# Kernel tuning notes

Hardware: AMD Instinct MI355X
Metric: run time of the kernel (lower is better)

Reference implementation:

```python
import jax, jax.numpy as jnp
import numpy as np

B, N, C, H = 8, 8192, 256, 8  # batch, tokens, dim, heads


def setup_inputs() -> dict:
    key = jax.random.key(0)
    ks = jax.random.split(key, 12)
    p = lambda i, shape: jax.random.normal(ks[i], shape, jnp.float32) * 0.02
    return {
        "x0": jax.random.normal(ks[0], (B, N, C), jnp.float32),
        "x1": jax.random.normal(ks[1], (B, N, C), jnp.float32),
        # relation_judger MLP (shared by both directions)
        "fc1_w": p(2, (C, 2 * C)), "fc1_b": jnp.zeros((C,), jnp.float32),
        "fc2_w": p(3, (C, C)), "fc2_b": jnp.zeros((C,), jnp.float32),
        # cross_attn_0_to_1
        "in_w_01": p(4, (3 * C, C)), "in_b_01": jnp.zeros((3 * C,), jnp.float32),
        "out_w_01": p(5, (C, C)), "out_b_01": jnp.zeros((C,), jnp.float32),
        # cross_attn_1_to_0
        "in_w_10": p(6, (3 * C, C)), "in_b_10": jnp.zeros((3 * C,), jnp.float32),
        "out_w_10": p(7, (C, C)), "out_b_10": jnp.zeros((C,), jnp.float32),
        # noise embeddings (2 rows each)
        "k_noise": p(8, (2, C)), "v_noise": p(9, (2, C)),
    }


def _judge(a, b, fc1_w, fc1_b, fc2_w, fc2_b):
    # Mlp2(2C->C->C) + softmax over channels; torch GELU default = exact erf
    h = jax.nn.gelu(jnp.concatenate([a, b], axis=-1) @ fc1_w.T + fc1_b, approximate=False)
    return jax.nn.softmax(h @ fc2_w.T + fc2_b, axis=-1)


def _mha_kv2(q, k, v, Wi, bi, Wo, bo):
    # q: [B,N,C]; k,v: [B,N,2,C]. Each token attends over its own 2 kv slots
    # (matches torch MHA with batch_first=False, seq_q=1, seq_kv=2, batch=N).
    hd = C // H
    Q = (q @ Wi[:C].T + bi[:C]).reshape(B, N, H, hd)
    K = (k @ Wi[C:2 * C].T + bi[C:2 * C]).reshape(B, N, 2, H, hd)
    V = (v @ Wi[2 * C:].T + bi[2 * C:]).reshape(B, N, 2, H, hd)
    scores = jnp.einsum('bnhd,bnkhd->bnhk', Q, K) / jnp.sqrt(jnp.asarray(hd, q.dtype))
    attn = jax.nn.softmax(scores, axis=-1)  # [B,N,H,2]
    ctx = jnp.einsum('bnhk,bnkhd->bnhd', attn, V).reshape(B, N, C)
    return ctx @ Wo.T + bo


def reference(x0, x1, fc1_w, fc1_b, fc2_w, fc2_b,
              in_w_01, in_b_01, out_w_01, out_b_01,
              in_w_10, in_b_10, out_w_10, out_b_10,
              k_noise, v_noise):
    # noise expansion was under @torch.no_grad() -> detach noise weights
    kn = jax.lax.stop_gradient(k_noise)
    vn = jax.lax.stop_gradient(v_noise)

    rel01 = _judge(x0, x1, fc1_w, fc1_b, fc2_w, fc2_b)       # [B,N,C]
    k01 = jnp.stack([x0 + kn[0], x0 * rel01], axis=2)        # [B,N,2,C]
    v01 = jnp.stack([x0 + vn[0], x1], axis=2)
    out01 = _mha_kv2(x0, k01, v01, in_w_01, in_b_01, out_w_01, out_b_01)

    rel10 = _judge(x1, x0, fc1_w, fc1_b, fc2_w, fc2_b)
    k10 = jnp.stack([x1 + kn[1], x1 * rel10], axis=2)
    v10 = jnp.stack([x1 + vn[1], x0], axis=2)
    out10 = _mha_kv2(x1, k10, v10, in_w_10, in_b_10, out_w_10, out_b_10)

    return x0 + out01, x1 + out10
```

## Files before the change

kernel.cpp:

```cpp
#include <hip/hip_runtime.h>
#include <cstdint>
#include <cstddef>


#define BNv  65536
#define TBNv 131072
#define NCv  16777216ull

typedef __attribute__((ext_vector_type(4))) float  f32x4;
typedef __attribute__((ext_vector_type(8))) short  short8;
typedef __attribute__((ext_vector_type(4))) float  float4_t;
typedef __attribute__((ext_vector_type(4))) unsigned short ushort4_t;

__device__ __forceinline__ float b2f(unsigned short u) {
  unsigned int x = ((unsigned int)u) << 16;
  return __builtin_bit_cast(float, x);
}
__device__ __forceinline__ unsigned short f2b(float f) {
  unsigned int u = __builtin_bit_cast(unsigned int, f);
  unsigned int r = (u + 0x7fffu + ((u >> 16) & 1u)) >> 16;
  return (unsigned short)r;
}

__device__ __forceinline__ void async16(const void* g, void* l) {
  __builtin_amdgcn_global_load_lds(
      (const __attribute__((address_space(1))) void*)g,
      (__attribute__((address_space(3))) void*)l, 16, 0, 0);
}

__device__ __forceinline__ void mfma_loop(
    const unsigned short* __restrict__ A1,
    const unsigned short* __restrict__ A2,
    const unsigned short* __restrict__ W,
    int ldw, int koff2, int npairs,
    size_t Arow0, int Wrow0,
    unsigned short* Asm, unsigned short* Wsm,
    f32x4 (&acc)[4][4], int t)
{
  const int l  = t & 63;
  const int wv = t >> 6;
  const int wr = (wv >> 1) * 64;
  const int wc = (wv & 1) * 64;
  const int lr = l & 15;
  const int kcS = (((l >> 4) ^ ((lr >> 1) & 3)) * 8);

  const int srow  = t >> 2;
  const int scolS = (((t & 3) ^ ((t >> 3) & 3)) * 8);
  const int ldst  = t * 8;

  for (int p = 0; p < npairs; ++p) {
    const unsigned short* A = p ? A2 : A1;
    const int kb = p ? koff2 : 0;
    for (int kt = 0; kt < 8; ++kt) {
      const int k0 = kt * 32;
      __syncthreads();
      async16(&A[(Arow0 + srow) * 256 + (size_t)(k0 + scolS)],        &Asm[ldst]);
      async16(&A[(Arow0 + 64 + srow) * 256 + (size_t)(k0 + scolS)],   &Asm[64 * 32 + ldst]);
      async16(&W[(size_t)(Wrow0 + srow) * ldw + (kb + k0 + scolS)],      &Wsm[ldst]);
      async16(&W[(size_t)(Wrow0 + 64 + srow) * ldw + (kb + k0 + scolS)], &Wsm[64 * 32 + ldst]);
      __syncthreads();

      short8 af[4], bfr[4];
#pragma unroll
      for (int m = 0; m < 4; ++m)
        af[m] = *(const short8*)&Asm[(wr + m * 16 + lr) * 32 + kcS];
#pragma unroll
      for (int n = 0; n < 4; ++n)
        bfr[n] = *(const short8*)&Wsm[(wc + n * 16 + lr) * 32 + kcS];
#pragma unroll
      for (int m = 0; m < 4; ++m)
#pragma unroll
        for (int n = 0; n < 4; ++n)
          acc[m][n] = __builtin_amdgcn_mfma_f32_16x16x32_bf16(af[m], bfr[n], acc[m][n], 0, 0, 0);
    }
  }
}

template <int EPI>
__device__ __forceinline__ void store_tile(
    f32x4 (&acc)[4][4], int t,
    const float* __restrict__ bias,
    const float* __restrict__ res,
    void* __restrict__ outp,
    int ldo)
{
  const int l = t & 63, wv = t >> 6;
  const int wr = (wv >> 1) * 64, wc = (wv & 1) * 64;
  const int lr = l & 15, lq = l >> 4;
#pragma unroll
  for (int m = 0; m < 4; ++m) {
#pragma unroll
    for (int n = 0; n < 4; ++n) {
#pragma unroll
      for (int r = 0; r < 4; ++r) {
        int rowi = wr + m * 16 + lq * 4 + r;
        int coli = wc + n * 16 + lr;
        float v = acc[m][n][r] + bias[coli];
        if (EPI == 1)
          v = 0.5f * v * (1.0f + erff(v * 0.70710678118654752f));
        if (EPI == 2)
          ((float*)outp)[(size_t)rowi * ldo + coli] = v + res[(size_t)rowi * 256 + coli];
        else
          ((unsigned short*)outp)[(size_t)rowi * ldo + coli] = f2b(v);
      }
    }
  }
}

__global__ __launch_bounds__(256)
void gemm_mega(const unsigned short* __restrict__ xb,
               const unsigned short* __restrict__ Wcat0,
               const unsigned short* __restrict__ Wcat1,
               const unsigned short* __restrict__ wfc1,
               const float* __restrict__ bcat0,
               const float* __restrict__ bcat1,
               const float* __restrict__ fc1_b,
               unsigned short* __restrict__ qkv,
               unsigned short* __restrict__ v1b,
               unsigned short* __restrict__ hbuf)
{
  __shared__ unsigned short Asm[128 * 32];
  __shared__ unsigned short Wsm[128 * 32];
  const int t = threadIdx.x;

  const int nwg = 10240, BPC = 160;
  int bid  = blockIdx.x;
  int wgid = (bid & 7) * (nwg >> 3) + (bid >> 3);
  int chunk = wgid / BPC, rem = wgid % BPC;
  int x = chunk * 16 + rem / 10;
  int y = rem % 10;

  const int half = x >> 9;
  const size_t tok0 = (size_t)(x & 511) * 128;
  const unsigned short* A1 = xb + (size_t)half * (BNv * 256);

  f32x4 acc[4][4] = {};

  if (y < 8) {
    const unsigned short* W = half ? Wcat1 : Wcat0;
    const float* bias = (half ? bcat1 : bcat0) + y * 128;
    mfma_loop(A1, nullptr, W, 256, 0, 1, tok0, y * 128, Asm, Wsm, acc, t);
    if (y < 6) {
      size_t row0 = (size_t)half * BNv + tok0;
      store_tile<0>(acc, t, bias, nullptr, qkv + row0 * 768 + y * 128, 768);
    } else {
      size_t row0 = (size_t)(1 - half) * BNv + tok0;
      store_tile<0>(acc, t, bias, nullptr, v1b + row0 * 256 + (y - 6) * 128, 256);
    }
  } else {
    const unsigned short* A2 = xb + (size_t)(1 - half) * (BNv * 256);
    mfma_loop(A1, A2, wfc1, 512, 256, 2, tok0, (y - 8) * 128, Asm, Wsm, acc, t);
    size_t row0 = (size_t)half * BNv + tok0;
    store_tile<1>(acc, t, fc1_b + (y - 8) * 128, nullptr,
                  hbuf + row0 * 256 + (y - 8) * 128, 256);
  }
}

template <int EPI>
__global__ __launch_bounds__(256)
void gemm_b2(const unsigned short* __restrict__ A,
             const unsigned short* __restrict__ W0,
             const unsigned short* __restrict__ W1,
             const float* __restrict__ b0, const float* __restrict__ b1,
             const float* __restrict__ res0, const float* __restrict__ res1,
             void* __restrict__ outp)
{
  __shared__ unsigned short Asm[128 * 32];
  __shared__ unsigned short Wsm[128 * 32];
  const int t = threadIdx.x;

  const int nwg = 2048;
  int bid  = blockIdx.x;
  int wgid = (bid & 7) * (nwg >> 3) + (bid >> 3);
  int chunk = wgid >> 5, rem = wgid & 31;
  int x = chunk * 16 + (rem >> 1);
  int y = rem & 1;

  const int half = x >> 9;
  const size_t row0 = (size_t)x * 128;

  f32x4 acc[4][4] = {};
  mfma_loop(A, nullptr, half ? W1 : W0, 256, 0, 1, row0, y * 128, Asm, Wsm, acc, t);

  const float* bias = (half ? b1 : b0) + y * 128;
  if (EPI == 2) {
    const float* res = (half ? res1 : res0) + (row0 - (size_t)half * BNv) * 256 + y * 128;
    store_tile<2>(acc, t, bias, res, (float*)outp + row0 * 256 + y * 128, 256);
  } else {
    store_tile<0>(acc, t, bias, nullptr,
                  (unsigned short*)outp + row0 * 256 + y * 128, 256);
  }
}


__global__ __launch_bounds__(256)
void cvt_x(const float* __restrict__ x0, const float* __restrict__ x1,
           unsigned short* __restrict__ xb)
{
  size_t i = ((size_t)blockIdx.x * 256 + threadIdx.x) * 8;
  const float* s = (i < NCv) ? (x0 + i) : (x1 + (i - NCv));
  float4_t a = *(const float4_t*)s;
  float4_t b = *(const float4_t*)(s + 4);
  short8 o;
  o[0] = (short)f2b(a[0]); o[1] = (short)f2b(a[1]);
  o[2] = (short)f2b(a[2]); o[3] = (short)f2b(a[3]);
  o[4] = (short)f2b(b[0]); o[5] = (short)f2b(b[1]);
  o[6] = (short)f2b(b[2]); o[7] = (short)f2b(b[3]);
  *(short8*)(xb + i) = o;
}

__global__ __launch_bounds__(256)
void prep_w(const float* fc1_w, const float* fc2_w,
            const float* in_w01, const float* out_w01,
            const float* in_w10, const float* out_w10,
            unsigned short* wfc1, unsigned short* wfc2,
            unsigned short* Wcat0, unsigned short* Wcat1,
            unsigned short* wout0, unsigned short* wout1)
{
  const float* src; unsigned short* dst; int n;
  switch (blockIdx.y) {
    case 0: src = fc1_w;             dst = wfc1;             n = 131072; break;
    case 1: src = fc2_w;             dst = wfc2;             n = 65536;  break;
    case 2: src = in_w01;            dst = Wcat0;            n = 196608; break;
    case 3: src = in_w10 + 512*256;  dst = Wcat0 + 768*256;  n = 65536;  break;
    case 4: src = in_w10;            dst = Wcat1;            n = 196608; break;
    case 5: src = in_w01 + 512*256;  dst = Wcat1 + 768*256;  n = 65536;  break;
    case 6: src = out_w01;           dst = wout0;            n = 65536;  break;
    default: src = out_w10;          dst = wout1;            n = 65536;  break;
  }
  int i = (blockIdx.x * 256 + threadIdx.x) * 4;
  if (i >= n) return;
  float4_t v = *(const float4_t*)(src + i);
  ushort4_t o;
  o[0] = f2b(v[0]); o[1] = f2b(v[1]); o[2] = f2b(v[2]); o[3] = f2b(v[3]);
  *(ushort4_t*)(dst + i) = o;
}

__global__ __launch_bounds__(256)
void prep_bcat(const float* in_w01, const float* in_b01,
               const float* in_w10, const float* in_b10,
               const float* kn, const float* vn,
               float* bcat0, float* bcat1)
{
  int j = blockIdx.x * 256 + threadIdx.x;
  int h = j >> 10, c = j & 1023;
  const float* inw  = h ? in_w10 : in_w01;
  const float* inb  = h ? in_b10 : in_b01;
  const float* oinb = h ? in_b01 : in_b10;
  float v;
  if (c < 256) v = inb[c];
  else if (c < 768) {
    const float* nz = (c < 512 ? kn : vn) + h * 256;
    const float* wrow = inw + (size_t)c * 256;
    float s = 0.f;
    for (int k = 0; k < 256; ++k) s += nz[k] * wrow[k];
    v = inb[c] + s;
  } else v = oinb[512 + (c - 768)];
  (h ? bcat1 : bcat0)[c] = v;
}

__global__ __launch_bounds__(256)
void softmax_mul(const unsigned short* __restrict__ s,
                 const unsigned short* __restrict__ xb,
                 unsigned short* __restrict__ k1in)
{
  size_t row = (size_t)blockIdx.x * 4 + (threadIdx.x >> 6);
  int l = threadIdx.x & 63;
  const unsigned short* p = s + row * 256;
  float v[4];
#pragma unroll
  for (int j = 0; j < 4; ++j) v[j] = b2f(p[l + 64 * j]);
  float mx = fmaxf(fmaxf(v[0], v[1]), fmaxf(v[2], v[3]));
#pragma unroll
  for (int off = 32; off > 0; off >>= 1) mx = fmaxf(mx, __shfl_xor(mx, off, 64));
  float sum = 0.f;
#pragma unroll
  for (int j = 0; j < 4; ++j) { v[j] = expf(v[j] - mx); sum += v[j]; }
#pragma unroll
  for (int off = 32; off > 0; off >>= 1) sum += __shfl_xor(sum, off, 64);
  float inv = 1.f / sum;
  const unsigned short* xr = xb + row * 256;
  unsigned short* o = k1in + row * 256;
#pragma unroll
  for (int j = 0; j < 4; ++j)
    o[l + 64 * j] = f2b(v[j] * inv * b2f(xr[l + 64 * j]));
}

__global__ __launch_bounds__(256)
void attn2(const unsigned short* __restrict__ qkv,
           const unsigned short* __restrict__ k1b,
           const unsigned short* __restrict__ v1b,
           unsigned short* __restrict__ ctx)
{
  int tid = blockIdx.x * 256 + threadIdx.x;
  size_t tok = (size_t)(tid >> 3);
  int h = tid & 7;
  const unsigned short* q   = qkv + tok * 768 + h * 32;
  const unsigned short* k0p = q + 256;
  const unsigned short* v0p = q + 512;
  const unsigned short* k1p = k1b + tok * 256 + h * 32;
  const unsigned short* v1p = v1b + tok * 256 + h * 32;
  unsigned short* op = ctx + tok * 256 + h * 32;

  float s0 = 0.f, s1 = 0.f;
#pragma unroll
  for (int c = 0; c < 4; ++c) {
    short8 q8 = *(const short8*)(q + c * 8);
    short8 a8 = *(const short8*)(k0p + c * 8);
    short8 b8 = *(const short8*)(k1p + c * 8);
#pragma unroll
    for (int j = 0; j < 8; ++j) {
      float qf = b2f((unsigned short)q8[j]);
      s0 += qf * b2f((unsigned short)a8[j]);
      s1 += qf * b2f((unsigned short)b8[j]);
    }
  }
  const float sc = 0.17677669529663687f;
  s0 *= sc; s1 *= sc;
  float mx = fmaxf(s0, s1);
  float e0 = expf(s0 - mx), e1 = expf(s1 - mx);
  float inv = 1.f / (e0 + e1);
  e0 *= inv; e1 *= inv;
#pragma unroll
  for (int c = 0; c < 4; ++c) {
    short8 a8 = *(const short8*)(v0p + c * 8);
    short8 b8 = *(const short8*)(v1p + c * 8);
    short8 o8;
#pragma unroll
    for (int j = 0; j < 8; ++j)
      o8[j] = (short)f2b(e0 * b2f((unsigned short)a8[j]) + e1 * b2f((unsigned short)b8[j]));
    *(short8*)(op + c * 8) = o8;
  }
}

extern "C" void kernel_launch(void* const* d_in, const int* in_sizes, int n_in,
                              void* d_out, int out_size, void* d_ws, size_t ws_size,
                              hipStream_t stream)
{
  const float* x0     = (const float*)d_in[0];
  const float* x1     = (const float*)d_in[1];
  const float* fc1_w  = (const float*)d_in[2];
  const float* fc1_b  = (const float*)d_in[3];
  const float* fc2_w  = (const float*)d_in[4];
  const float* fc2_b  = (const float*)d_in[5];
  const float* in_w01 = (const float*)d_in[6];
  const float* in_b01 = (const float*)d_in[7];
  const float* out_w01= (const float*)d_in[8];
  const float* out_b01= (const float*)d_in[9];
  const float* in_w10 = (const float*)d_in[10];
  const float* in_b10 = (const float*)d_in[11];
  const float* out_w10= (const float*)d_in[12];
  const float* out_b10= (const float*)d_in[13];
  const float* kn     = (const float*)d_in[14];
  const float* vn     = (const float*)d_in[15];

  char* ws = (char*)d_ws;
  unsigned short* xb   = (unsigned short*)ws; ws += TBNv * 256 * 2;
  unsigned short* qkv  = (unsigned short*)ws; ws += (size_t)TBNv * 768 * 2;
  unsigned short* v1b  = (unsigned short*)ws; ws += TBNv * 256 * 2;
  unsigned short* hbuf = (unsigned short*)ws; ws += TBNv * 256 * 2;
  unsigned short* sbuf = (unsigned short*)ws; ws += TBNv * 256 * 2;
  unsigned short* wfc1 = (unsigned short*)ws; ws += 131072 * 2;
  unsigned short* wfc2 = (unsigned short*)ws; ws += 65536 * 2;
  unsigned short* Wcat0= (unsigned short*)ws; ws += 262144 * 2;
  unsigned short* Wcat1= (unsigned short*)ws; ws += 262144 * 2;
  unsigned short* wout0= (unsigned short*)ws; ws += 65536 * 2;
  unsigned short* wout1= (unsigned short*)ws; ws += 65536 * 2;
  float* bcat0 = (float*)ws; ws += 1024 * 4;
  float* bcat1 = (float*)ws; ws += 1024 * 4;

  unsigned short* k1in = hbuf;
  unsigned short* k1b  = sbuf;
  unsigned short* ctx  = xb;

  if (ws_size < (size_t)(ws - (char*)d_ws)) return;

  dim3 blk(256);

  cvt_x<<<16384, blk, 0, stream>>>(x0, x1, xb);
  prep_w<<<dim3(192, 8), blk, 0, stream>>>(fc1_w, fc2_w, in_w01, out_w01,
                                           in_w10, out_w10,
                                           wfc1, wfc2, Wcat0, Wcat1, wout0, wout1);
  prep_bcat<<<8, blk, 0, stream>>>(in_w01, in_b01, in_w10, in_b10, kn, vn,
                                   bcat0, bcat1);
  gemm_mega<<<10240, blk, 0, stream>>>(xb, Wcat0, Wcat1, wfc1,
                                       bcat0, bcat1, fc1_b, qkv, v1b, hbuf);
  gemm_b2<0><<<2048, blk, 0, stream>>>(hbuf, wfc2, wfc2, fc2_b, fc2_b,
                                       nullptr, nullptr, sbuf);
  softmax_mul<<<32768, blk, 0, stream>>>(sbuf, xb, k1in);
  gemm_b2<0><<<2048, blk, 0, stream>>>(k1in, Wcat0 + 256 * 256, Wcat1 + 256 * 256,
                                       in_b01 + 256, in_b10 + 256,
                                       nullptr, nullptr, k1b);
  attn2<<<4096, blk, 0, stream>>>(qkv, k1b, v1b, ctx);
  gemm_b2<2><<<2048, blk, 0, stream>>>(ctx, wout0, wout1, out_b01, out_b10,
                                       x0, x1, d_out);
}
```

Before: 751.8 us.

## Double-buffer LDS tiles in GEMM main loop and hoist bias loads

Doubles the shared-memory A/W tiles so the async global-to-LDS copy for the next K step is issued before computing on the current buffer. This drops one barrier per step and is meant to overlap memory latency with MFMA work. Bias values are preloaded into registers before the main loop instead of being read per element in the epilogue. Launch bounds now request 4 blocks per CU. The cost is twice the LDS per block, which may limit occupancy. The overlap only happens if the async copy's completion wait is not forced to drain right away.

```diff
diff --git a/kernel.cpp b/kernel.cpp
--- a/kernel.cpp
+++ b/kernel.cpp
@@ -48,38 +48,53 @@
   const int scolS = (((t & 3) ^ ((t >> 3) & 3)) * 8);
   const int ldst  = t * 8;
 
-  for (int p = 0; p < npairs; ++p) {
-    const unsigned short* A = p ? A2 : A1;
-    const int kb = p ? koff2 : 0;
-    for (int kt = 0; kt < 8; ++kt) {
-      const int k0 = kt * 32;
-      __syncthreads();
-      async16(&A[(Arow0 + srow) * 256 + (size_t)(k0 + scolS)],        &Asm[ldst]);
-      async16(&A[(Arow0 + 64 + srow) * 256 + (size_t)(k0 + scolS)],   &Asm[64 * 32 + ldst]);
-      async16(&W[(size_t)(Wrow0 + srow) * ldw + (kb + k0 + scolS)],      &Wsm[ldst]);
-      async16(&W[(size_t)(Wrow0 + 64 + srow) * ldw + (kb + k0 + scolS)], &Wsm[64 * 32 + ldst]);
-      __syncthreads();
-
-      short8 af[4], bfr[4];
-#pragma unroll
-      for (int m = 0; m < 4; ++m)
-        af[m] = *(const short8*)&Asm[(wr + m * 16 + lr) * 32 + kcS];
+  const int nsteps = npairs * 8;
+
+  auto stage = [&](int s, int bsel) {
+    const unsigned short* A = (s >= 8) ? A2 : A1;
+    const int kb = (s >= 8) ? koff2 : 0;
+    const int k0 = (s & 7) * 32;
+    unsigned short* Ab = Asm + bsel * (128 * 32);
+    unsigned short* Wb = Wsm + bsel * (128 * 32);
+    async16(&A[(Arow0 + srow) * 256 + (size_t)(k0 + scolS)],        &Ab[ldst]);
+    async16(&A[(Arow0 + 64 + srow) * 256 + (size_t)(k0 + scolS)],   &Ab[64 * 32 + ldst]);
+    async16(&W[(size_t)(Wrow0 + srow) * ldw + (kb + k0 + scolS)],      &Wb[ldst]);
+    async16(&W[(size_t)(Wrow0 + 64 + srow) * ldw + (kb + k0 + scolS)], &Wb[64 * 32 + ldst]);
+  };
+
+  stage(0, 0);
+  for (int s = 0; s < nsteps; ++s) {
+    __syncthreads();
+    if (s + 1 < nsteps) stage(s + 1, (s + 1) & 1);
+    const unsigned short* Ab = Asm + (s & 1) * (128 * 32);
+    const unsigned short* Wb = Wsm + (s & 1) * (128 * 32);
+    short8 af[4], bfr[4];
+#pragma unroll
+    for (int m = 0; m < 4; ++m)
+      af[m] = *(const short8*)&Ab[(wr + m * 16 + lr) * 32 + kcS];
+#pragma unroll
+    for (int n = 0; n < 4; ++n)
+      bfr[n] = *(const short8*)&Wb[(wc + n * 16 + lr) * 32 + kcS];
+#pragma unroll
+    for (int m = 0; m < 4; ++m)
 #pragma unroll
       for (int n = 0; n < 4; ++n)
-        bfr[n] = *(const short8*)&Wsm[(wc + n * 16 + lr) * 32 + kcS];
-#pragma unroll
-      for (int m = 0; m < 4; ++m)
-#pragma unroll
-        for (int n = 0; n < 4; ++n)
-          acc[m][n] = __builtin_amdgcn_mfma_f32_16x16x32_bf16(af[m], bfr[n], acc[m][n], 0, 0, 0);
-    }
-  }
+        acc[m][n] = __builtin_amdgcn_mfma_f32_16x16x32_bf16(af[m], bfr[n], acc[m][n], 0, 0, 0);
+  }
+}
+
+__device__ __forceinline__ void load_bias4(const float* __restrict__ bias,
+                                           int t, float (&b4)[4])
+{
+  const int l = t & 63, wv = t >> 6;
+  const int wc = (wv & 1) * 64, lr = l & 15;
+#pragma unroll
+  for (int n = 0; n < 4; ++n) b4[n] = bias[wc + n * 16 + lr];
 }
 
 template <int EPI>
 __device__ __forceinline__ void store_tile(
-    f32x4 (&acc)[4][4], int t,
-    const float* __restrict__ bias,
+    f32x4 (&acc)[4][4], int t, const float (&b4)[4],
     const float* __restrict__ res,
     void* __restrict__ outp,
     int ldo)
@@ -95,7 +110,7 @@
       for (int r = 0; r < 4; ++r) {
         int rowi = wr + m * 16 + lq * 4 + r;
         int coli = wc + n * 16 + lr;
-        float v = acc[m][n][r] + bias[coli];
+        float v = acc[m][n][r] + b4[n];
         if (EPI == 1)
           v = 0.5f * v * (1.0f + erff(v * 0.70710678118654752f));
         if (EPI == 2)
@@ -107,7 +122,7 @@
   }
 }
 
-__global__ __launch_bounds__(256)
+__global__ __launch_bounds__(256, 4)
 void gemm_mega(const unsigned short* __restrict__ xb,
                const unsigned short* __restrict__ Wcat0,
                const unsigned short* __restrict__ Wcat1,
@@ -119,8 +134,8 @@
                unsigned short* __restrict__ v1b,
                unsigned short* __restrict__ hbuf)
 {
-  __shared__ unsigned short Asm[128 * 32];
-  __shared__ unsigned short Wsm[128 * 32];
+  __shared__ unsigned short Asm[2 * 128 * 32];
+  __shared__ unsigned short Wsm[2 * 128 * 32];
   const int t = threadIdx.x;
 
   const int nwg = 10240, BPC = 160;
@@ -135,29 +150,30 @@
   const unsigned short* A1 = xb + (size_t)half * (BNv * 256);
 
   f32x4 acc[4][4] = {};
+  float b4[4];
 
   if (y < 8) {
     const unsigned short* W = half ? Wcat1 : Wcat0;
-    const float* bias = (half ? bcat1 : bcat0) + y * 128;
+    load_bias4((half ? bcat1 : bcat0) + y * 128, t, b4);
     mfma_loop(A1, nullptr, W, 256, 0, 1, tok0, y * 128, Asm, Wsm, acc, t);
     if (y < 6) {
       size_t row0 = (size_t)half * BNv + tok0;
-      store_tile<0>(acc, t, bias, nullptr, qkv + row0 * 768 + y * 128, 768);
+      store_tile<0>(acc, t, b4, nullptr, qkv + row0 * 768 + y * 128, 768);
     } else {
       size_t row0 = (size_t)(1 - half) * BNv + tok0;
-      store_tile<0>(acc, t, bias, nullptr, v1b + row0 * 256 + (y - 6) * 128, 256);
+      store_tile<0>(acc, t, b4, nullptr, v1b + row0 * 256 + (y - 6) * 128, 256);
     }
   } else {
     const unsigned short* A2 = xb + (size_t)(1 - half) * (BNv * 256);
+    load_bias4(fc1_b + (y - 8) * 128, t, b4);
     mfma_loop(A1, A2, wfc1, 512, 256, 2, tok0, (y - 8) * 128, Asm, Wsm, acc, t);
     size_t row0 = (size_t)half * BNv + tok0;
-    store_tile<1>(acc, t, fc1_b + (y - 8) * 128, nullptr,
-                  hbuf + row0 * 256 + (y - 8) * 128, 256);
+    store_tile<1>(acc, t, b4, nullptr, hbuf + row0 * 256 + (y - 8) * 128, 256);
   }
 }
 
 template <int EPI>
-__global__ __launch_bounds__(256)
+__global__ __launch_bounds__(256, 4)
 void gemm_b2(const unsigned short* __restrict__ A,
              const unsigned short* __restrict__ W0,
              const unsigned short* __restrict__ W1,
@@ -165,8 +181,8 @@
              const float* __restrict__ res0, const float* __restrict__ res1,
              void* __restrict__ outp)
 {
-  __shared__ unsigned short Asm[128 * 32];
-  __shared__ unsigned short Wsm[128 * 32];
+  __shared__ unsigned short Asm[2 * 128 * 32];
+  __shared__ unsigned short Wsm[2 * 128 * 32];
   const int t = threadIdx.x;
 
   const int nwg = 2048;
@@ -180,14 +196,15 @@
   const size_t row0 = (size_t)x * 128;
 
   f32x4 acc[4][4] = {};
+  float b4[4];
+  load_bias4((half ? b1 : b0) + y * 128, t, b4);
   mfma_loop(A, nullptr, half ? W1 : W0, 256, 0, 1, row0, y * 128, Asm, Wsm, acc, t);
 
-  const float* bias = (half ? b1 : b0) + y * 128;
   if (EPI == 2) {
     const float* res = (half ? res1 : res0) + (row0 - (size_t)half * BNv) * 256 + y * 128;
-    store_tile<2>(acc, t, bias, res, (float*)outp + row0 * 256 + y * 128, 256);
+    store_tile<2>(acc, t, b4, res, (float*)outp + row0 * 256 + y * 128, 256);
   } else {
-    store_tile<0>(acc, t, bias, nullptr,
+    store_tile<0>(acc, t, b4, nullptr,
                   (unsigned short*)outp + row0 * 256 + y * 128, 256);
   }
 }
```

Result: no change. 754.9 us (+0.4%).
